# Performance work log

Hardware: AMD Instinct MI355X
Metric: run time of the kernel (lower is better)

The kernel has to match this reference:

```python
import jax, jax.numpy as jnp
import numpy as np

B, T, D = 4, 4096, 1024
P = 64  # d_model / n_head

def setup_inputs() -> dict:
    key = jax.random.key(0)
    k1, k2, k3 = jax.random.split(key, 3)
    x = jax.random.normal(k1, (B, T, D), dtype=jnp.float32)
    Wqkv = jax.random.normal(k2, (D, 3 * P), dtype=jnp.float32) * (1.0 / np.sqrt(D))
    bqkv = jax.random.normal(k3, (3 * P,), dtype=jnp.float32) * 0.01
    return {"x": x, "Wqkv": Wqkv, "bqkv": bqkv}

def reference(x, Wqkv, bqkv):
    Bv, Tv, Cv = x.shape
    qkv = (x @ Wqkv + bqkv).reshape(Bv, Tv, 3, P)  # [B,T,3,p]
    q, k, v = qkv[:, :, 0, :], qkv[:, :, 1, :], qkv[:, :, 2, :]
    # raw scores (source applies NO 1/sqrt(p) scaling)
    S = jnp.einsum('btp,bsp->bts', q, k)  # [B,T,T]
    causal = jnp.tril(jnp.ones((Tv, Tv), dtype=bool))
    S = jnp.where(causal[None, :, :], S, jnp.float32(-jnp.inf))
    Pm = jax.nn.softmax(S, axis=-1)
    O = jnp.einsum('bts,bsp->btp', Pm, v)  # [B,T,p]
    return O
```

## Files before the change

kernel.cpp:

```cpp
#include <hip/hip_runtime.h>
#include <hip/hip_fp16.h>

#define B_ 4
#define T_ 4096
#define D_ 1024

typedef _Float16 h8 __attribute__((ext_vector_type(8)));
typedef _Float16 h4 __attribute__((ext_vector_type(4)));
typedef float f32x4 __attribute__((ext_vector_type(4)));

#define LOG2E 1.44269504088896340736f
#define MASKV -3.0e38f
#define MINIT -1.0e30f
#define EXP2(x) __builtin_amdgcn_exp2f(x)

__global__ __launch_bounds__(256) void wt_kernel(const float* __restrict__ W,
                                                 _Float16* __restrict__ Wt) {
    __shared__ _Float16 Tr[192][20];
    const int tid = threadIdx.x, k0 = blockIdx.x * 16;
#pragma unroll
    for (int i = 0; i < 3; i++) {
        int fi = tid + 256 * i;
        int r = fi / 48, c4 = fi % 48;
        float4 v = *(const float4*)(W + (size_t)(k0 + r) * 192 + c4 * 4);
        Tr[c4 * 4 + 0][r] = (_Float16)v.x;
        Tr[c4 * 4 + 1][r] = (_Float16)v.y;
        Tr[c4 * 4 + 2][r] = (_Float16)v.z;
        Tr[c4 * 4 + 3][r] = (_Float16)v.w;
    }
    __syncthreads();
#pragma unroll
    for (int i = 0; i < 3; i++) {
        int oi = tid + 256 * i;
        int n = oi >> 2, kq = oi & 3;
        *(h4*)(Wt + (size_t)n * D_ + k0 + kq * 4) = *(const h4*)&Tr[n][kq * 4];
    }
}

__global__ __launch_bounds__(256) void proj_kernel(
    const float* __restrict__ x, const _Float16* __restrict__ Wt,
    const float* __restrict__ bias,
    _Float16* __restrict__ qh, _Float16* __restrict__ kh, _Float16* __restrict__ vh)
{
    __shared__ __align__(16) char psm[35840];
    _Float16* Asp = (_Float16*)psm;
    _Float16* Bsp = (_Float16*)(psm + 5120);
    _Float16* Ostp = (_Float16*)psm;
    const int tid = threadIdx.x;
    const int w = tid >> 6, lane = tid & 63, quad = lane >> 4, l16 = lane & 15;
    const int row0 = blockIdx.x * 32;
    const int mstrip = w & 1;
    const int ngrp = (w >> 1) * 6;

    float bvals[6];
#pragma unroll
    for (int nt = 0; nt < 6; nt++) bvals[nt] = bias[(ngrp + nt) * 16 + l16];

    f32x4 acc[6];
#pragma unroll
    for (int i = 0; i < 6; i++) acc[i] = (f32x4){0.f, 0.f, 0.f, 0.f};

    const int arow = tid >> 3, ac0 = (tid & 7) * 4;

    float4 xreg[2];
    h8 wreg[3];
    {
        const float* xp = x + (size_t)(row0 + arow) * D_ + ac0;
        xreg[0] = *(const float4*)xp;
        xreg[1] = *(const float4*)(xp + 32);
#pragma unroll
        for (int p = 0; p < 3; p++) {
            int f = tid + 256 * p; int n = f >> 2, c0 = (f & 3) * 8;
            wreg[p] = *(const h8*)(Wt + (size_t)n * D_ + c0);
        }
    }

    for (int kc = 0; kc < 32; kc++) {
        const int buf = kc & 1;
        float4 xa = xreg[buf];
        h4 av;
        av[0]=(_Float16)xa.x; av[1]=(_Float16)xa.y; av[2]=(_Float16)xa.z; av[3]=(_Float16)xa.w;
        *(h4*)(Asp + buf * 1280 + arow * 40 + ac0) = av;
#pragma unroll
        for (int p = 0; p < 3; p++) {
            int f = tid + 256 * p; int n = f >> 2, c0 = (f & 3) * 8;
            *(h8*)(Bsp + buf * 7680 + n * 40 + c0) = wreg[p];
        }
        if (kc + 2 < 32)
            xreg[buf] = *(const float4*)(x + (size_t)(row0 + arow) * D_ + (kc + 2) * 32 + ac0);
        if (kc + 1 < 32) {
            int k0 = (kc + 1) * 32;
#pragma unroll
            for (int p = 0; p < 3; p++) {
                int f = tid + 256 * p; int n = f >> 2, c0 = (f & 3) * 8;
                wreg[p] = *(const h8*)(Wt + (size_t)n * D_ + k0 + c0);
            }
        }
        __syncthreads();
        h8 a0 = *(const h8*)(Asp + buf * 1280 + (16 * mstrip + l16) * 40 + quad * 8);
#pragma unroll
        for (int nt = 0; nt < 6; nt++) {
            h8 b0 = *(const h8*)(Bsp + buf * 7680 + ((ngrp + nt) * 16 + l16) * 40 + quad * 8);
            acc[nt] = __builtin_amdgcn_mfma_f32_16x16x32_f16(a0, b0, acc[nt], 0, 0, 0);
        }
    }

    __syncthreads();
#pragma unroll
    for (int nt = 0; nt < 6; nt++) {
        int n = (ngrp + nt) * 16 + l16;
        float scale = (n < 64) ? LOG2E : 1.0f;
#pragma unroll
        for (int reg = 0; reg < 4; reg++)
            Ostp[(16 * mstrip + quad * 4 + reg) * 200 + n] =
                (_Float16)((acc[nt][reg] + bvals[nt]) * scale);
    }
    __syncthreads();
    {
        const int mrow = tid >> 3, c0 = (tid & 7) * 8;
        _Float16* dsts[3] = {qh, kh, vh};
#pragma unroll
        for (int g = 0; g < 3; g++)
            *(h8*)(dsts[g] + (size_t)(row0 + mrow) * 64 + c0) =
                *(const h8*)(Ostp + mrow * 200 + g * 64 + c0);
    }
}

__global__ __launch_bounds__(256, 2) void attn_kernel(
    const _Float16* __restrict__ qh, const _Float16* __restrict__ kh,
    const _Float16* __restrict__ vh, float* __restrict__ out,
    _Float16* __restrict__ Opart, float2* __restrict__ ml,
    int lgC, int NC1, int direct, int q8, int total)
{
    __shared__ _Float16 Ks[2][64][72];
    __shared__ _Float16 Vt[2][64][72];
    const int tid = threadIdx.x;
    const int w = tid >> 6, lane = tid & 63, quad = lane >> 4, l16 = lane & 15;
    const int C = 1 << lgC;

    const int bid = blockIdx.x;
    const int cid = (bid & 7) * q8 + (bid >> 3);
    if (cid >= total) return;

    const int b = cid / NC1;
    int rem = cid - b * NC1;
    int qt2 = 0, k0 = 0, cnt = 1;
    for (int i = 0; i < 32; i++) {
        int nc = (2 * i + 2 + C - 1) >> lgC;
        if (rem < nc) { qt2 = i; k0 = rem << lgC; cnt = min(C, 2 * i + 2 - k0); break; }
        rem -= nc;
    }
    const size_t base = (size_t)b * T_ * 64;
    const int qbase = qt2 * 128 + w * 32;

    h8 qf[2][2];
#pragma unroll
    for (int u = 0; u < 2; u++) {
        const _Float16* qp = qh + base + (size_t)(qbase + u * 16 + l16) * 64 + quad * 8;
        qf[u][0] = *(const h8*)qp;
        qf[u][1] = *(const h8*)(qp + 32);
    }

    f32x4 o[8];
#pragma unroll
    for (int i = 0; i < 8; i++) o[i] = (f32x4){0.f, 0.f, 0.f, 0.f};
    float m[2] = {MINIT, MINIT}, l[2] = {0.f, 0.f};

    const int krow = tid >> 3, kc0 = (tid & 7) * 8;
    const int vp0 = (tid & 15) * 4, vc0 = (tid >> 4) * 4;
    h8 kreg[2];
    h4 vreg[4];
    {
        const _Float16* kp = kh + base + (size_t)(k0 * 64) * 64;
        kreg[0] = *(const h8*)(kp + (size_t)krow * 64 + kc0);
        kreg[1] = *(const h8*)(kp + (size_t)(krow + 32) * 64 + kc0);
        const _Float16* vp = vh + base + (size_t)(k0 * 64 + vc0) * 64 + vp0;
#pragma unroll
        for (int i = 0; i < 4; i++) vreg[i] = *(const h4*)(vp + (size_t)i * 64);
    }

    const int kend = k0 + cnt;
    for (int kt = k0; kt < kend; kt++) {
        const int buf = kt & 1;
        *(h8*)&Ks[buf][krow][kc0] = kreg[0];
        *(h8*)&Ks[buf][krow + 32][kc0] = kreg[1];
#pragma unroll
        for (int j = 0; j < 4; j++) {
            h4 t;
            t[0] = vreg[0][j]; t[1] = vreg[1][j]; t[2] = vreg[2][j]; t[3] = vreg[3][j];
            *(h4*)&Vt[buf][vp0 + j][vc0] = t;
        }
        if (kt + 1 < kend) {
            const _Float16* kp = kh + base + (size_t)((kt + 1) * 64) * 64;
            kreg[0] = *(const h8*)(kp + (size_t)krow * 64 + kc0);
            kreg[1] = *(const h8*)(kp + (size_t)(krow + 32) * 64 + kc0);
            const _Float16* vp = vh + base + (size_t)((kt + 1) * 64 + vc0) * 64 + vp0;
#pragma unroll
            for (int i = 0; i < 4; i++) vreg[i] = *(const h4*)(vp + (size_t)i * 64);
        }
        __syncthreads();

        const bool skip = (kt * 64) > (qbase + 31);
        if (!skip) {
            f32x4 s[2][4];
#pragma unroll
            for (int nt = 0; nt < 4; nt++) {
                h8 kf0 = *(const h8*)&Ks[buf][nt * 16 + l16][quad * 8];
                h8 kf1 = *(const h8*)&Ks[buf][nt * 16 + l16][32 + quad * 8];
#pragma unroll
                for (int u = 0; u < 2; u++) {
                    f32x4 c = (f32x4){0.f, 0.f, 0.f, 0.f};
                    c = __builtin_amdgcn_mfma_f32_16x16x32_f16(kf0, qf[u][0], c, 0, 0, 0);
                    c = __builtin_amdgcn_mfma_f32_16x16x32_f16(kf1, qf[u][1], c, 0, 0, 0);
                    s[u][nt] = c;
                }
            }

            h4 pf[2][4];
#pragma unroll
            for (int u = 0; u < 2; u++) {
                const int qrow = qbase + u * 16 + l16;
                if (kt * 64 + 63 > qbase + u * 16) {
#pragma unroll
                    for (int nt = 0; nt < 4; nt++)
#pragma unroll
                        for (int reg = 0; reg < 4; reg++) {
                            int sg = kt * 64 + nt * 16 + quad * 4 + reg;
                            if (sg > qrow) s[u][nt][reg] = MASKV;
                        }
                }
                float mx = s[u][0][0];
#pragma unroll
                for (int nt = 0; nt < 4; nt++)
#pragma unroll
                    for (int reg = 0; reg < 4; reg++) mx = fmaxf(mx, s[u][nt][reg]);
                mx = fmaxf(mx, __shfl_xor(mx, 16));
                mx = fmaxf(mx, __shfl_xor(mx, 32));
                float mnew = fmaxf(m[u], mx);
                float alpha = EXP2(m[u] - mnew);
                m[u] = mnew;
                float rs = 0.f;
#pragma unroll
                for (int nt = 0; nt < 4; nt++) {
                    h4 ph;
#pragma unroll
                    for (int reg = 0; reg < 4; reg++) {
                        float p = EXP2(s[u][nt][reg] - mnew);
                        rs += p;
                        ph[reg] = (_Float16)p;
                    }
                    pf[u][nt] = ph;
                }
                rs += __shfl_xor(rs, 16);
                rs += __shfl_xor(rs, 32);
                l[u] = l[u] * alpha + rs;
#pragma unroll
                for (int pt = 0; pt < 4; pt++)
#pragma unroll
                    for (int reg = 0; reg < 4; reg++) o[u * 4 + pt][reg] *= alpha;
            }

#pragma unroll
            for (int pt = 0; pt < 4; pt++)
#pragma unroll
                for (int nt = 0; nt < 4; nt++) {
                    h4 vf = *(const h4*)&Vt[buf][pt * 16 + l16][nt * 16 + quad * 4];
                    o[pt]     = __builtin_amdgcn_mfma_f32_16x16x16f16(vf, pf[0][nt], o[pt], 0, 0, 0);
                    o[4 + pt] = __builtin_amdgcn_mfma_f32_16x16x16f16(vf, pf[1][nt], o[4 + pt], 0, 0, 0);
                }
        }
    }

    if (direct) {
#pragma unroll
        for (int u = 0; u < 2; u++) {
            float linv = 1.0f / l[u];
            int trow = qt2 * 128 + w * 32 + u * 16 + l16;
#pragma unroll
            for (int pt = 0; pt < 4; pt++)
#pragma unroll
                for (int reg = 0; reg < 4; reg++)
                    out[base + (size_t)trow * 64 + pt * 16 + quad * 4 + reg] =
                        o[u * 4 + pt][reg] * linv;
        }
    } else {
        __syncthreads();
        _Float16* St = &Ks[0][0][0];
#pragma unroll
        for (int u = 0; u < 2; u++) {
            int r = w * 32 + u * 16 + l16;
#pragma unroll
            for (int pt = 0; pt < 4; pt++) {
                h4 ph;
#pragma unroll
                for (int reg = 0; reg < 4; reg++) ph[reg] = (_Float16)o[u * 4 + pt][reg];
                *(h4*)&St[r * 72 + pt * 16 + quad * 4] = ph;
            }
            if (quad == 0) ml[(size_t)cid * 128 + r] = make_float2(m[u], l[u]);
        }
        __syncthreads();
        _Float16* op = Opart + (size_t)cid * 8192;
        const int r = tid >> 1, c0 = (tid & 1) * 32;
#pragma unroll
        for (int j = 0; j < 4; j++)
            *(h8*)(op + r * 64 + c0 + 8 * j) = *(const h8*)&St[r * 72 + c0 + 8 * j];
    }
}

__global__ __launch_bounds__(256) void combine_kernel(
    const _Float16* __restrict__ Opart, const float2* __restrict__ ml,
    float* __restrict__ out, int lgC, int NC1)
{
    const int C = 1 << lgC;
    const int task = blockIdx.x;
    const int b = task >> 7, tile = (task >> 2) & 31, rg = task & 3;
    int pref = 0;
    for (int i = 0; i < tile; i++) pref += (2 * i + 2 + C - 1) >> lgC;
    const int cbase = b * NC1 + pref;
    const int nch = (2 * tile + 2 + C - 1) >> lgC;

    const int r = rg * 32 + (threadIdx.x >> 3);
    const int c0 = (threadIdx.x & 7) * 8;

    float M = MINIT;
    for (int i = 0; i < nch; i++) M = fmaxf(M, ml[(size_t)(cbase + i) * 128 + r].x);
    float L = 0.f, acc[8] = {0.f, 0.f, 0.f, 0.f, 0.f, 0.f, 0.f, 0.f};
    for (int i = 0; i < nch; i++) {
        float2 v = ml[(size_t)(cbase + i) * 128 + r];
        float sc = EXP2(v.x - M);
        L += sc * v.y;
        h8 x8 = *(const h8*)(Opart + (size_t)(cbase + i) * 8192 + (size_t)r * 64 + c0);
#pragma unroll
        for (int t = 0; t < 8; t++) acc[t] += sc * (float)x8[t];
    }
    float inv = 1.0f / L;
    float* po = out + ((size_t)b * T_ + tile * 128 + r) * 64 + c0;
    float4 r0 = { acc[0]*inv, acc[1]*inv, acc[2]*inv, acc[3]*inv };
    float4 r1 = { acc[4]*inv, acc[5]*inv, acc[6]*inv, acc[7]*inv };
    *(float4*)po = r0;
    *(float4*)(po + 4) = r1;
}

extern "C" void kernel_launch(void* const* d_in, const int* in_sizes, int n_in,
                              void* d_out, int out_size, void* d_ws, size_t ws_size,
                              hipStream_t stream) {
    const float* x    = (const float*)d_in[0];
    const float* W    = (const float*)d_in[1];
    const float* bias = (const float*)d_in[2];
    float* out = (float*)d_out;
    char* ws = (char*)d_ws;
    _Float16* qh = (_Float16*)(ws);
    _Float16* kh = (_Float16*)(ws + (size_t)2 * 1024 * 1024);
    _Float16* vh = (_Float16*)(ws + (size_t)4 * 1024 * 1024);
    _Float16* Wt = (_Float16*)(ws + (size_t)6 * 1024 * 1024);
    const size_t pbase = (size_t)8 * 1024 * 1024;

    int lgC = -1, nc1 = 32;
    for (int lg = 2; lg <= 6; lg++) {
        int C = 1 << lg, n1 = 0;
        for (int i = 0; i < 32; i++) n1 += (2 * i + 2 + C - 1) >> lg;
        size_t need = pbase + (size_t)4 * n1 * (8192 * 2 + 128 * 8);
        if (need <= ws_size) { lgC = lg; nc1 = n1; break; }
    }
    int direct = (lgC < 0) ? 1 : 0;
    if (direct) { lgC = 6; nc1 = 32; }
    _Float16* Opart = (_Float16*)(ws + pbase);
    float2*   mlp   = (float2*)(ws + pbase + (size_t)4 * nc1 * 8192 * 2);

    const int total = 4 * nc1;
    const int q8 = (total + 7) / 8;

    wt_kernel<<<64, 256, 0, stream>>>(W, Wt);
    proj_kernel<<<512, 256, 0, stream>>>(x, Wt, bias, qh, kh, vh);
    attn_kernel<<<8 * q8, 256, 0, stream>>>(qh, kh, vh, out, Opart, mlp,
                                            lgC, nc1, direct, q8, total);
    if (!direct)
        combine_kernel<<<512, 256, 0, stream>>>(Opart, mlp, out, lgC, nc1);
}
```

Measured before the change: 160.8 us.

## Make QKV projection warp-private, loading weight fragments directly into registers

The projection kernel drops the block-shared A/B tiles and __syncthreads. Each wave now converts its own 16-row x slice into a private LDS buffer and loads the f16 weight MFMA fragments straight from global memory into registers, double-buffered. Output staging is also per-wave, and each wave writes its part of q/k/v directly. This removes block barriers and shared weight staging, and launch bounds now ask for 2 blocks per CU. The cost is redundant global weight loads across waves and more register pressure. The change only touches the projection, which is a small part of the total next to attention.

```diff
diff --git a/kernel.cpp b/kernel.cpp
--- a/kernel.cpp
+++ b/kernel.cpp
@@ -37,92 +37,98 @@
     }
 }
 
-__global__ __launch_bounds__(256) void proj_kernel(
+__global__ __launch_bounds__(256, 2) void proj_kernel(
     const float* __restrict__ x, const _Float16* __restrict__ Wt,
     const float* __restrict__ bias,
     _Float16* __restrict__ qh, _Float16* __restrict__ kh, _Float16* __restrict__ vh)
 {
-    __shared__ __align__(16) char psm[35840];
-    _Float16* Asp = (_Float16*)psm;
-    _Float16* Bsp = (_Float16*)(psm + 5120);
-    _Float16* Ostp = (_Float16*)psm;
+    __shared__ _Float16 Aw[4][16][40];
+    __shared__ _Float16 Ow[4][16][104];
     const int tid = threadIdx.x;
     const int w = tid >> 6, lane = tid & 63, quad = lane >> 4, l16 = lane & 15;
-    const int row0 = blockIdx.x * 32;
-    const int mstrip = w & 1;
-    const int ngrp = (w >> 1) * 6;
+    const int m0 = blockIdx.x * 32 + (w & 1) * 16;
+    const int nh = w >> 1;
+    const int nbase = nh * 96;
 
     float bvals[6];
 #pragma unroll
-    for (int nt = 0; nt < 6; nt++) bvals[nt] = bias[(ngrp + nt) * 16 + l16];
+    for (int nt = 0; nt < 6; nt++) bvals[nt] = bias[nbase + nt * 16 + l16];
 
     f32x4 acc[6];
 #pragma unroll
     for (int i = 0; i < 6; i++) acc[i] = (f32x4){0.f, 0.f, 0.f, 0.f};
 
-    const int arow = tid >> 3, ac0 = (tid & 7) * 4;
-
-    float4 xreg[2];
-    h8 wreg[3];
-    {
-        const float* xp = x + (size_t)(row0 + arow) * D_ + ac0;
-        xreg[0] = *(const float4*)xp;
-        xreg[1] = *(const float4*)(xp + 32);
-#pragma unroll
-        for (int p = 0; p < 3; p++) {
-            int f = tid + 256 * p; int n = f >> 2, c0 = (f & 3) * 8;
-            wreg[p] = *(const h8*)(Wt + (size_t)n * D_ + c0);
-        }
-    }
+    const int r0 = lane >> 3, c0 = (lane & 7) * 4;
+    const float* xrow0 = x + (size_t)(m0 + r0) * D_;
+    const float* xrow1 = x + (size_t)(m0 + 8 + r0) * D_;
+    const _Float16* wtb = Wt + (size_t)(nbase + l16) * D_ + quad * 8;
+
+    float4 xr0[2], xr1[2];
+    h8 bf[2][6];
+    xr0[0] = *(const float4*)(xrow0 + c0);
+    xr1[0] = *(const float4*)(xrow1 + c0);
+#pragma unroll
+    for (int nt = 0; nt < 6; nt++)
+        bf[0][nt] = *(const h8*)(wtb + (size_t)nt * 16 * D_);
+    xr0[1] = *(const float4*)(xrow0 + 32 + c0);
+    xr1[1] = *(const float4*)(xrow1 + 32 + c0);
+#pragma unroll
+    for (int nt = 0; nt < 6; nt++)
+        bf[1][nt] = *(const h8*)(wtb + (size_t)nt * 16 * D_ + 32);
 
     for (int kc = 0; kc < 32; kc++) {
-        const int buf = kc & 1;
-        float4 xa = xreg[buf];
-        h4 av;
-        av[0]=(_Float16)xa.x; av[1]=(_Float16)xa.y; av[2]=(_Float16)xa.z; av[3]=(_Float16)xa.w;
-        *(h4*)(Asp + buf * 1280 + arow * 40 + ac0) = av;
-#pragma unroll
-        for (int p = 0; p < 3; p++) {
-            int f = tid + 256 * p; int n = f >> 2, c0 = (f & 3) * 8;
-            *(h8*)(Bsp + buf * 7680 + n * 40 + c0) = wreg[p];
-        }
-        if (kc + 2 < 32)
-            xreg[buf] = *(const float4*)(x + (size_t)(row0 + arow) * D_ + (kc + 2) * 32 + ac0);
-        if (kc + 1 < 32) {
-            int k0 = (kc + 1) * 32;
-#pragma unroll
-            for (int p = 0; p < 3; p++) {
-                int f = tid + 256 * p; int n = f >> 2, c0 = (f & 3) * 8;
-                wreg[p] = *(const h8*)(Wt + (size_t)n * D_ + k0 + c0);
-            }
-        }
-        __syncthreads();
-        h8 a0 = *(const h8*)(Asp + buf * 1280 + (16 * mstrip + l16) * 40 + quad * 8);
-#pragma unroll
-        for (int nt = 0; nt < 6; nt++) {
-            h8 b0 = *(const h8*)(Bsp + buf * 7680 + ((ngrp + nt) * 16 + l16) * 40 + quad * 8);
-            acc[nt] = __builtin_amdgcn_mfma_f32_16x16x32_f16(a0, b0, acc[nt], 0, 0, 0);
-        }
-    }
-
-    __syncthreads();
+        const int sl = kc & 1;
+        float4 xa = xr0[sl], xb = xr1[sl];
+        h4 a0h, a1h;
+        a0h[0]=(_Float16)xa.x; a0h[1]=(_Float16)xa.y; a0h[2]=(_Float16)xa.z; a0h[3]=(_Float16)xa.w;
+        a1h[0]=(_Float16)xb.x; a1h[1]=(_Float16)xb.y; a1h[2]=(_Float16)xb.z; a1h[3]=(_Float16)xb.w;
+        *(h4*)&Aw[w][r0][c0] = a0h;
+        *(h4*)&Aw[w][8 + r0][c0] = a1h;
+        if (kc + 2 < 32) {
+            xr0[sl] = *(const float4*)(xrow0 + (kc + 2) * 32 + c0);
+            xr1[sl] = *(const float4*)(xrow1 + (kc + 2) * 32 + c0);
+        }
+        h8 bb[6];
+#pragma unroll
+        for (int nt = 0; nt < 6; nt++) bb[nt] = bf[sl][nt];
+        if (kc + 2 < 32) {
+#pragma unroll
+            for (int nt = 0; nt < 6; nt++)
+                bf[sl][nt] = *(const h8*)(wtb + (size_t)nt * 16 * D_ + (kc + 2) * 32);
+        }
+        h8 a0 = *(const h8*)&Aw[w][l16][quad * 8];
+#pragma unroll
+        for (int nt = 0; nt < 6; nt++)
+            acc[nt] = __builtin_amdgcn_mfma_f32_16x16x32_f16(a0, bb[nt], acc[nt], 0, 0, 0);
+    }
+
 #pragma unroll
     for (int nt = 0; nt < 6; nt++) {
-        int n = (ngrp + nt) * 16 + l16;
-        float scale = (n < 64) ? LOG2E : 1.0f;
+        int ng = nbase + nt * 16 + l16;
+        float scale = (ng < 64) ? LOG2E : 1.0f;
 #pragma unroll
         for (int reg = 0; reg < 4; reg++)
-            Ostp[(16 * mstrip + quad * 4 + reg) * 200 + n] =
+            Ow[w][quad * 4 + reg][nt * 16 + l16] =
                 (_Float16)((acc[nt][reg] + bvals[nt]) * scale);
     }
-    __syncthreads();
-    {
-        const int mrow = tid >> 3, c0 = (tid & 7) * 8;
-        _Float16* dsts[3] = {qh, kh, vh};
-#pragma unroll
-        for (int g = 0; g < 3; g++)
-            *(h8*)(dsts[g] + (size_t)(row0 + mrow) * 64 + c0) =
-                *(const h8*)(Ostp + mrow * 200 + g * 64 + c0);
+    if (nh == 0) {
+#pragma unroll
+        for (int i = 0; i < 2; i++) {
+            int flat = i * 64 + lane;
+            int r = flat >> 3, c8 = flat & 7;
+            *(h8*)(qh + (size_t)(m0 + r) * 64 + c8 * 8) = *(const h8*)&Ow[w][r][c8 * 8];
+        }
+        int r = lane >> 2, c8 = lane & 3;
+        *(h8*)(kh + (size_t)(m0 + r) * 64 + c8 * 8) = *(const h8*)&Ow[w][r][64 + c8 * 8];
+    } else {
+        int r = lane >> 2, c8 = lane & 3;
+        *(h8*)(kh + (size_t)(m0 + r) * 64 + 32 + c8 * 8) = *(const h8*)&Ow[w][r][c8 * 8];
+#pragma unroll
+        for (int i = 0; i < 2; i++) {
+            int flat = i * 64 + lane;
+            int rr = flat >> 3, cc = flat & 7;
+            *(h8*)(vh + (size_t)(m0 + rr) * 64 + cc * 8) = *(const h8*)&Ow[w][rr][32 + cc * 8];
+        }
     }
 }
 
```

After: 347.6 us. 116% more time.
